# Kernel optimization log

Measured on AMD Instinct MI355X. Metric: run time of the kernel, lower is better.

## Reference

```python
import jax, jax.numpy as jnp
import numpy as np

HIDDEN = 1024
FFN = 4096
NUM_EXPERTS = 8
TOP_K = 2
LOAD_BALANCE_WEIGHT = 0.01


def setup_inputs() -> dict:
    key = jax.random.key(0)
    ks = jax.random.split(key, 6)
    B, S = 4, 2048
    x = jax.random.normal(ks[0], (B, S, HIDDEN), dtype=jnp.float32)
    router_w = jax.random.normal(ks[1], (NUM_EXPERTS, HIDDEN), dtype=jnp.float32) * 0.02
    fc1_w = jax.random.normal(ks[2], (NUM_EXPERTS, FFN, HIDDEN), dtype=jnp.float32) * 0.02
    fc1_b = jnp.zeros((NUM_EXPERTS, FFN), dtype=jnp.float32)
    fc2_w = jax.random.normal(ks[3], (NUM_EXPERTS, HIDDEN, FFN), dtype=jnp.float32) * 0.02
    fc2_b = jnp.zeros((NUM_EXPERTS, HIDDEN), dtype=jnp.float32)
    return {"x": x, "router_w": router_w, "fc1_w": fc1_w, "fc1_b": fc1_b,
            "fc2_w": fc2_w, "fc2_b": fc2_b}


def reference(x, router_w, fc1_w, fc1_b, fc2_w, fc2_b):
    B, S, H = x.shape
    xf = x.reshape(-1, H)                       # [T, H]
    T = xf.shape[0]
    logits = xf @ router_w.T                    # [T, E]
    probs = jax.nn.softmax(logits, axis=-1)
    weights, indices = jax.lax.top_k(probs, TOP_K)   # [T, K]
    weights = weights / jnp.sum(weights, axis=-1, keepdims=True)
    # combine weight per (token, expert): sum of top-k weights assigned to expert
    onehot = jax.nn.one_hot(indices, NUM_EXPERTS, dtype=xf.dtype)  # [T, K, E]
    combine = jnp.sum(weights[..., None] * onehot, axis=1)          # [T, E]
    out = jnp.zeros_like(xf)
    for e in range(NUM_EXPERTS):
        h = jax.nn.gelu(xf @ fc1_w[e].T + fc1_b[e], approximate=False)
        y = h @ fc2_w[e].T + fc2_b[e]
        # tokens not routed to expert e have combine weight 0 -> contribute 0,
        # matching the torch masked gather/scatter-add exactly (dropout in eval).
        out = out + y * combine[:, e:e + 1]
    # load-balance aux loss
    counts = jnp.sum(onehot, axis=(0, 1))                # bincount of indices
    freq = counts / (T * TOP_K)
    aux_loss = LOAD_BALANCE_WEIGHT * NUM_EXPERTS * jnp.sum(jnp.mean(probs, axis=0) * freq)
    return out.reshape(B, S, H), aux_loss
```

## Files before the change

### kernel.cpp

```cpp
#include <hip/hip_runtime.h>
#include <math.h>

#define T_TOK 8192
#define HID 1024
#define FFN_DIM 4096
#define NEXP 8
#define BM 128
#define MAX_TILES 136

typedef __attribute__((ext_vector_type(8))) __bf16 bf16x8;
typedef __attribute__((ext_vector_type(8))) unsigned short ushort8;
typedef __attribute__((ext_vector_type(4))) float f32x4;

static __device__ __forceinline__ unsigned short f2bf(float f) {
  unsigned u = __builtin_bit_cast(unsigned, f);
  u += 0x7FFFu + ((u >> 16) & 1u);
  return (unsigned short)(u >> 16);
}

static __device__ __forceinline__ void gl16(const void* g, void* l) {
  __builtin_amdgcn_global_load_lds((const __attribute__((address_space(1))) unsigned int*)g,
                                   (__attribute__((address_space(3))) unsigned int*)l,
                                   16, 0, 0);
}

static __device__ __forceinline__ ushort8 cvt8(const float* p) {
  float4 a = *(const float4*)p, b = *(const float4*)(p + 4);
  ushort8 o;
  o[0] = f2bf(a.x); o[1] = f2bf(a.y); o[2] = f2bf(a.z); o[3] = f2bf(a.w);
  o[4] = f2bf(b.x); o[5] = f2bf(b.y); o[6] = f2bf(b.z); o[7] = f2bf(b.w);
  return o;
}

__global__ void moe_cvt_x(const float* __restrict__ x, unsigned short* __restrict__ xb) {
  size_t i = ((size_t)blockIdx.x * 256 + threadIdx.x) * 8;
  *(ushort8*)(xb + i) = cvt8(x + i);
}

__global__ void moe_cvt_w(const float* __restrict__ w1, const float* __restrict__ w2,
                          unsigned short* __restrict__ w1b, unsigned short* __restrict__ w2b) {
  size_t i = ((size_t)blockIdx.x * 256 + threadIdx.x) * 8;
  if (blockIdx.y == 0) *(ushort8*)(w1b + i) = cvt8(w1 + i);
  else                 *(ushort8*)(w2b + i) = cvt8(w2 + i);
}

__global__ void moe_router(const float* __restrict__ x, const float* __restrict__ rw,
                           int* __restrict__ tok_idx, float* __restrict__ tok_w,
                           float* __restrict__ pbuf) {
  int t = blockIdx.x * 4 + (threadIdx.x >> 6);
  int lane = threadIdx.x & 63;
  const float* xr = x + (size_t)t * HID;
  double acc[NEXP];
#pragma unroll
  for (int e = 0; e < NEXP; ++e) acc[e] = 0.0;
  for (int i = 0; i < HID / 64; ++i) {
    float xv = xr[lane + 64 * i];
#pragma unroll
    for (int e = 0; e < NEXP; ++e)
      acc[e] += (double)xv * (double)rw[e * HID + lane + 64 * i];
  }
#pragma unroll
  for (int off = 32; off; off >>= 1)
#pragma unroll
    for (int e = 0; e < NEXP; ++e) acc[e] += __shfl_xor(acc[e], off);
  if (lane == 0) {
    double m = acc[0];
#pragma unroll
    for (int e = 1; e < NEXP; ++e) m = acc[e] > m ? acc[e] : m;
    float pf[NEXP], s = 0.0f;
#pragma unroll
    for (int e = 0; e < NEXP; ++e) { pf[e] = expf((float)(acc[e] - m)); s += pf[e]; }
    int i0 = 0;
#pragma unroll
    for (int e = 1; e < NEXP; ++e) if (acc[e] > acc[i0]) i0 = e;
    int i1 = (i0 == 0) ? 1 : 0;
#pragma unroll
    for (int e = 0; e < NEXP; ++e) if (e != i0 && acc[e] > acc[i1]) i1 = e;
    float w0 = pf[i0], w1 = pf[i1], wsum = w0 + w1;
    tok_idx[2 * t] = i0; tok_idx[2 * t + 1] = i1;
    tok_w[2 * t] = w0 / wsum; tok_w[2 * t + 1] = w1 / wsum;
    float inv = 1.0f / s;
#pragma unroll
    for (int e = 0; e < NEXP; ++e) pbuf[(size_t)t * NEXP + e] = pf[e] * inv;
  }
}

__global__ void moe_scatter(const int* __restrict__ tok_idx, const float* __restrict__ tok_w,
                            int* __restrict__ cursor, int* __restrict__ list,
                            float* __restrict__ listw) {
  const int e = blockIdx.x;
  __shared__ int wsum[16];
  __shared__ int base;
  const int tid = threadIdx.x, lane = tid & 63, wv = tid >> 6;
  if (tid == 0) base = 0;
  __syncthreads();
  for (int c = 0; c < 2 * T_TOK; c += 1024) {
    int i = c + tid;
    int m = (tok_idx[i] == e) ? 1 : 0;
    unsigned long long bal = __ballot(m);
    if (lane == 0) wsum[wv] = __popcll(bal);
    __syncthreads();
    int wbase = base;
    for (int k = 0; k < wv; ++k) wbase += wsum[k];
    if (m) {
      int pos = wbase + __popcll(bal & ((1ull << lane) - 1ull));
      list[e * T_TOK + pos] = i >> 1;
      listw[e * T_TOK + pos] = tok_w[i];
    }
    __syncthreads();
    if (tid == 0) {
      int s = 0;
#pragma unroll
      for (int k = 0; k < 16; ++k) s += wsum[k];
      base += s;
    }
    __syncthreads();
  }
  if (tid == 0) cursor[e] = base;
}

__global__ void moe_preduce(const float* __restrict__ pbuf, float* __restrict__ probs_sum) {
  const int e = blockIdx.x;
  float s = 0.0f;
  for (int t = threadIdx.x; t < T_TOK; t += 256) s += pbuf[(size_t)t * NEXP + e];
  __shared__ float red[4];
#pragma unroll
  for (int off = 32; off; off >>= 1) s += __shfl_down(s, off);
  if ((threadIdx.x & 63) == 0) red[threadIdx.x >> 6] = s;
  __syncthreads();
  if (threadIdx.x == 0) probs_sum[e] = red[0] + red[1] + red[2] + red[3];
}

__global__ void moe_offsets(const int* __restrict__ cursor, int* __restrict__ offs,
                            int* __restrict__ tile_e, int* __restrict__ tile_m,
                            int* __restrict__ meta) {
  if (threadIdx.x == 0 && blockIdx.x == 0) {
    int o = 0, t = 0;
    for (int e = 0; e < NEXP; ++e) {
      offs[e] = o;
      int ntl = (cursor[e] + BM - 1) / BM;
      for (int k = 0; k < ntl; ++k) { tile_e[t] = e; tile_m[t] = k; ++t; }
      o += ntl * BM;
    }
    offs[NEXP] = o;
    meta[0] = t;
  }
}

__global__ __launch_bounds__(256, 4) void moe_fc1(
    const unsigned short* __restrict__ xb, const unsigned short* __restrict__ w1b,
    const float* __restrict__ b1, const int* __restrict__ list,
    const int* __restrict__ offs, const int* __restrict__ tile_e,
    const int* __restrict__ tile_m, const int* __restrict__ meta,
    unsigned short* __restrict__ hbuf, int cb, int ch) {
  const int bid = blockIdx.x;
  const int c = bid & 7;
  const int k = bid >> 3;
  const int tl = c * 17 + k % 17;
  const int nt = k / 17;
  if (tl >= meta[0]) return;
  const int e = tile_e[tl], mt = tile_m[tl];
  __shared__ __align__(16) char As[BM * 128];
  __shared__ __align__(16) char Bs[BM * 128];
  const int tid = threadIdx.x, lane = tid & 63, wv = tid >> 6;
  const int wr = wv >> 1, wc = wv & 1;
  const int swz = ((lane & 7) ^ (lane >> 3)) << 4;
  const int rsub = lane >> 3;
  const int* le = list + e * T_TOK + mt * BM;
  const char* asrc[4]; const char* bsrc[4];
  char* adst[4]; char* bdst[4];
#pragma unroll
  for (int j = 0; j < 4; ++j) {
    int r = wv * 32 + j * 8 + rsub;
    int tok = le[r]; tok = tok < 0 ? 0 : tok;
    asrc[j] = (const char*)(xb + (size_t)tok * HID) + swz;
    bsrc[j] = (const char*)(w1b + ((size_t)e * FFN_DIM + cb + nt * BM + r) * HID) + swz;
    adst[j] = As + (wv * 32 + j * 8) * 128;
    bdst[j] = Bs + (wv * 32 + j * 8) * 128;
  }
  f32x4 acc[4][4] = {};
  for (int kt = 0; kt < 16; ++kt) {
    if (kt) __syncthreads();
#pragma unroll
    for (int j = 0; j < 4; ++j) {
      gl16(asrc[j] + kt * 128, adst[j]);
      gl16(bsrc[j] + kt * 128, bdst[j]);
    }
    __syncthreads();
#pragma unroll
    for (int kh = 0; kh < 2; ++kh) {
      bf16x8 afr[4], bfr[4];
      const int kb = kh * 64 + ((lane >> 4) << 4);
#pragma unroll
      for (int m = 0; m < 4; ++m) {
        int row = wr * 64 + m * 16 + (lane & 15);
        afr[m] = *(const bf16x8*)(As + row * 128 + (kb ^ ((row & 7) << 4)));
      }
#pragma unroll
      for (int n = 0; n < 4; ++n) {
        int col = wc * 64 + n * 16 + (lane & 15);
        bfr[n] = *(const bf16x8*)(Bs + col * 128 + (kb ^ ((col & 7) << 4)));
      }
#pragma unroll
      for (int m = 0; m < 4; ++m)
#pragma unroll
        for (int n = 0; n < 4; ++n)
          acc[m][n] = __builtin_amdgcn_mfma_f32_16x16x32_bf16(afr[m], bfr[n], acc[m][n], 0, 0, 0);
    }
  }
  const float* b1e = b1 + (size_t)e * FFN_DIM + cb + nt * BM;
  const size_t rbase = (size_t)(offs[e] + mt * BM);
#pragma unroll
  for (int n = 0; n < 4; ++n) {
    int cl = wc * 64 + n * 16 + (lane & 15);
    float bias = b1e[cl];
#pragma unroll
    for (int m = 0; m < 4; ++m)
#pragma unroll
      for (int j = 0; j < 4; ++j) {
        int rl = wr * 64 + m * 16 + ((lane >> 4) << 2) + j;
        float v = acc[m][n][j] + bias;
        float g = 0.5f * v * (1.0f + erff(v * 0.70710678118654752f));
        hbuf[(rbase + rl) * ch + nt * BM + cl] = f2bf(g);
      }
  }
}

__global__ __launch_bounds__(256, 4) void moe_fc2(
    const unsigned short* __restrict__ hbuf, const unsigned short* __restrict__ w2b,
    const float* __restrict__ b2, const int* __restrict__ list, const float* __restrict__ listw,
    const int* __restrict__ offs, const int* __restrict__ tile_e,
    const int* __restrict__ tile_m, const int* __restrict__ meta,
    float* __restrict__ out, int cb, int ch) {
  const int bid = blockIdx.x;
  const int c = bid & 7;
  const int k = bid >> 3;
  const int tl = c * 17 + (k >> 3);
  const int nt = k & 7;
  if (tl >= meta[0]) return;
  const int e = tile_e[tl], mt = tile_m[tl];
  __shared__ __align__(16) char As[BM * 128];
  __shared__ __align__(16) char Bs[BM * 128];
  const int tid = threadIdx.x, lane = tid & 63, wv = tid >> 6;
  const int wr = wv >> 1, wc = wv & 1;
  const int swz = ((lane & 7) ^ (lane >> 3)) << 4;
  const int rsub = lane >> 3;
  const size_t rbase = (size_t)(offs[e] + mt * BM);
  const char* asrc[4]; const char* bsrc[4];
  char* adst[4]; char* bdst[4];
#pragma unroll
  for (int j = 0; j < 4; ++j) {
    int r = wv * 32 + j * 8 + rsub;
    asrc[j] = (const char*)(hbuf + (rbase + r) * ch) + swz;
    bsrc[j] = (const char*)(w2b + ((size_t)e * HID + nt * BM + r) * FFN_DIM + cb) + swz;
    adst[j] = As + (wv * 32 + j * 8) * 128;
    bdst[j] = Bs + (wv * 32 + j * 8) * 128;
  }
  f32x4 acc[4][4] = {};
  const int nK = ch / 64;
  for (int kt = 0; kt < nK; ++kt) {
    if (kt) __syncthreads();
#pragma unroll
    for (int j = 0; j < 4; ++j) {
      gl16(asrc[j] + kt * 128, adst[j]);
      gl16(bsrc[j] + kt * 128, bdst[j]);
    }
    __syncthreads();
#pragma unroll
    for (int kh = 0; kh < 2; ++kh) {
      bf16x8 afr[4], bfr[4];
      const int kb = kh * 64 + ((lane >> 4) << 4);
#pragma unroll
      for (int m = 0; m < 4; ++m) {
        int row = wr * 64 + m * 16 + (lane & 15);
        afr[m] = *(const bf16x8*)(As + row * 128 + (kb ^ ((row & 7) << 4)));
      }
#pragma unroll
      for (int n = 0; n < 4; ++n) {
        int col = wc * 64 + n * 16 + (lane & 15);
        bfr[n] = *(const bf16x8*)(Bs + col * 128 + (kb ^ ((col & 7) << 4)));
      }
#pragma unroll
      for (int m = 0; m < 4; ++m)
#pragma unroll
        for (int n = 0; n < 4; ++n)
          acc[m][n] = __builtin_amdgcn_mfma_f32_16x16x32_bf16(afr[m], bfr[n], acc[m][n], 0, 0, 0);
    }
  }
  const int* le = list + e * T_TOK + mt * BM;
  const float* lw = listw + e * T_TOK + mt * BM;
  const float* b2e = b2 + (size_t)e * HID + nt * BM;
#pragma unroll
  for (int m = 0; m < 4; ++m)
#pragma unroll
    for (int j = 0; j < 4; ++j) {
      int rl = wr * 64 + m * 16 + ((lane >> 4) << 2) + j;
      int tok = le[rl];
      if (tok < 0) continue;
      float wgt = lw[rl];
      float* orow = out + (size_t)tok * HID + nt * BM;
#pragma unroll
      for (int n = 0; n < 4; ++n) {
        int cl = wc * 64 + n * 16 + (lane & 15);
        float v = acc[m][n][j];
        if (cb == 0) v += b2e[cl];
        atomicAdd(orow + cl, wgt * v);
      }
    }
}

__global__ void moe_finalize(const float* __restrict__ probs_sum, const int* __restrict__ cursor,
                             float* __restrict__ out_aux) {
  if (threadIdx.x == 0 && blockIdx.x == 0) {
    float a = 0.0f;
    for (int e = 0; e < NEXP; ++e)
      a += (probs_sum[e] / (float)T_TOK) * ((float)cursor[e] / (float)(T_TOK * 2));
    out_aux[0] = 0.01f * (float)NEXP * a;
  }
}

extern "C" void kernel_launch(void* const* d_in, const int* in_sizes, int n_in,
                              void* d_out, int out_size, void* d_ws, size_t ws_size,
                              hipStream_t stream) {
  const float* x  = (const float*)d_in[0];
  const float* rw = (const float*)d_in[1];
  const float* w1 = (const float*)d_in[2];
  const float* b1 = (const float*)d_in[3];
  const float* w2 = (const float*)d_in[4];
  const float* b2 = (const float*)d_in[5];
  float* out = (float*)d_out;

  char* ws = (char*)d_ws;
  float* probs_sum = (float*)(ws + 0);
  int*   cursor    = (int*)(ws + 256);
  int*   meta      = (int*)(ws + 512);
  int*   offs      = (int*)(ws + 1024);
  int*   tile_e    = (int*)(ws + 2048);
  int*   tile_m    = (int*)(ws + 4096);
  int*   tok_idx   = (int*)(ws + 8192);
  float* tok_w     = (float*)(ws + 8192 + 65536);
  int*   list      = (int*)(ws + 8192 + 131072);
  float* listw     = (float*)(ws + 8192 + 393216);
  float* pbuf      = (float*)(ws + 8192 + 655360);
  unsigned short* xb   = (unsigned short*)(ws + 1048576);
  unsigned short* w1be = (unsigned short*)(ws + 17825792);
  unsigned short* w2be = (unsigned short*)(ws + 84934656);
  const size_t HBUF_OFF = 152043520;
  unsigned short* hbuf = (unsigned short*)(ws + HBUF_OFF);

  int CH = 4096;
  while (CH > 1024 && HBUF_OFF + (size_t)(MAX_TILES * BM) * CH * 2 > ws_size) CH >>= 1;

  hipMemsetAsync(d_out, 0, (size_t)out_size * sizeof(float), stream);
  hipMemsetAsync(ws + 8192 + 131072, 0xFF, 262144, stream);

  moe_cvt_x<<<4096, 256, 0, stream>>>(x, xb);
  moe_cvt_w<<<dim3(16384, 2), 256, 0, stream>>>(w1, w2, w1be, w2be);
  moe_router<<<T_TOK / 4, 256, 0, stream>>>(x, rw, tok_idx, tok_w, pbuf);
  moe_scatter<<<NEXP, 1024, 0, stream>>>(tok_idx, tok_w, cursor, list, listw);
  moe_preduce<<<NEXP, 256, 0, stream>>>(pbuf, probs_sum);
  moe_offsets<<<1, 1, 0, stream>>>(cursor, offs, tile_e, tile_m, meta);

  for (int cb = 0; cb < FFN_DIM; cb += CH) {
    moe_fc1<<<MAX_TILES * (CH / BM), 256, 0, stream>>>(
        xb, w1be, b1, list, offs, tile_e, tile_m, meta, hbuf, cb, CH);
    moe_fc2<<<MAX_TILES * 8, 256, 0, stream>>>(
        hbuf, w2be, b2, list, listw, offs, tile_e, tile_m, meta, out, cb, CH);
  }
  moe_finalize<<<1, 64, 0, stream>>>(probs_sum, cursor, out + (size_t)T_TOK * HID);
}
```

Measured before the change: 665.9 us.

## Replace fc2 atomic scatter with dense expert output buffer and gather combine

fc2 now writes each expert row's result plainly into a per-expert-row fp32 buffer instead of atomically adding weighted results into the output. A new combine kernel gathers each token's two expert rows through an inverse index and applies the routing weights. The x-to-bf16 conversion is also folded into the router kernel, and the output memset is dropped. This trades atomic contention for an extra ~100MB of buffer traffic and a larger workspace.

```diff
diff --git a/kernel.cpp b/kernel.cpp
--- a/kernel.cpp
+++ b/kernel.cpp
@@ -32,11 +32,6 @@
   return o;
 }
 
-__global__ void moe_cvt_x(const float* __restrict__ x, unsigned short* __restrict__ xb) {
-  size_t i = ((size_t)blockIdx.x * 256 + threadIdx.x) * 8;
-  *(ushort8*)(xb + i) = cvt8(x + i);
-}
-
 __global__ void moe_cvt_w(const float* __restrict__ w1, const float* __restrict__ w2,
                           unsigned short* __restrict__ w1b, unsigned short* __restrict__ w2b) {
   size_t i = ((size_t)blockIdx.x * 256 + threadIdx.x) * 8;
@@ -46,15 +41,17 @@
 
 __global__ void moe_router(const float* __restrict__ x, const float* __restrict__ rw,
                            int* __restrict__ tok_idx, float* __restrict__ tok_w,
-                           float* __restrict__ pbuf) {
+                           float* __restrict__ pbuf, unsigned short* __restrict__ xb) {
   int t = blockIdx.x * 4 + (threadIdx.x >> 6);
   int lane = threadIdx.x & 63;
   const float* xr = x + (size_t)t * HID;
+  unsigned short* xbr = xb + (size_t)t * HID;
   double acc[NEXP];
 #pragma unroll
   for (int e = 0; e < NEXP; ++e) acc[e] = 0.0;
   for (int i = 0; i < HID / 64; ++i) {
     float xv = xr[lane + 64 * i];
+    xbr[lane + 64 * i] = f2bf(xv);
 #pragma unroll
     for (int e = 0; e < NEXP; ++e)
       acc[e] += (double)xv * (double)rw[e * HID + lane + 64 * i];
@@ -85,9 +82,9 @@
   }
 }
 
-__global__ void moe_scatter(const int* __restrict__ tok_idx, const float* __restrict__ tok_w,
+__global__ void moe_scatter(const int* __restrict__ tok_idx,
                             int* __restrict__ cursor, int* __restrict__ list,
-                            float* __restrict__ listw) {
+                            int* __restrict__ inv) {
   const int e = blockIdx.x;
   __shared__ int wsum[16];
   __shared__ int base;
@@ -105,7 +102,7 @@
     if (m) {
       int pos = wbase + __popcll(bal & ((1ull << lane) - 1ull));
       list[e * T_TOK + pos] = i >> 1;
-      listw[e * T_TOK + pos] = tok_w[i];
+      inv[i] = (e << 13) | pos;
     }
     __syncthreads();
     if (tid == 0) {
@@ -228,10 +225,9 @@
 
 __global__ __launch_bounds__(256, 4) void moe_fc2(
     const unsigned short* __restrict__ hbuf, const unsigned short* __restrict__ w2b,
-    const float* __restrict__ b2, const int* __restrict__ list, const float* __restrict__ listw,
-    const int* __restrict__ offs, const int* __restrict__ tile_e,
-    const int* __restrict__ tile_m, const int* __restrict__ meta,
-    float* __restrict__ out, int cb, int ch) {
+    const float* __restrict__ b2, const int* __restrict__ offs,
+    const int* __restrict__ tile_e, const int* __restrict__ tile_m,
+    const int* __restrict__ meta, float* __restrict__ ybuf, int cb, int ch) {
   const int bid = blockIdx.x;
   const int c = bid & 7;
   const int k = bid >> 3;
@@ -287,26 +283,40 @@
           acc[m][n] = __builtin_amdgcn_mfma_f32_16x16x32_bf16(afr[m], bfr[n], acc[m][n], 0, 0, 0);
     }
   }
-  const int* le = list + e * T_TOK + mt * BM;
-  const float* lw = listw + e * T_TOK + mt * BM;
   const float* b2e = b2 + (size_t)e * HID + nt * BM;
 #pragma unroll
   for (int m = 0; m < 4; ++m)
 #pragma unroll
     for (int j = 0; j < 4; ++j) {
       int rl = wr * 64 + m * 16 + ((lane >> 4) << 2) + j;
-      int tok = le[rl];
-      if (tok < 0) continue;
-      float wgt = lw[rl];
-      float* orow = out + (size_t)tok * HID + nt * BM;
+      float* yrow = ybuf + (rbase + rl) * HID + nt * BM;
 #pragma unroll
       for (int n = 0; n < 4; ++n) {
         int cl = wc * 64 + n * 16 + (lane & 15);
         float v = acc[m][n][j];
-        if (cb == 0) v += b2e[cl];
-        atomicAdd(orow + cl, wgt * v);
-      }
-    }
+        if (cb == 0) yrow[cl] = v + b2e[cl];
+        else         yrow[cl] += v;
+      }
+    }
+}
+
+__global__ void moe_combine(const float* __restrict__ ybuf, const int* __restrict__ inv,
+                            const float* __restrict__ tok_w, const int* __restrict__ offs,
+                            float* __restrict__ out) {
+  const int t = blockIdx.x;
+  const int col = threadIdx.x * 4;
+  int v0 = inv[2 * t], v1 = inv[2 * t + 1];
+  size_t r0 = (size_t)(offs[v0 >> 13] + (v0 & 8191));
+  size_t r1 = (size_t)(offs[v1 >> 13] + (v1 & 8191));
+  float w0 = tok_w[2 * t], w1 = tok_w[2 * t + 1];
+  float4 a = *(const float4*)(ybuf + r0 * HID + col);
+  float4 b = *(const float4*)(ybuf + r1 * HID + col);
+  float4 o;
+  o.x = w0 * a.x + w1 * b.x;
+  o.y = w0 * a.y + w1 * b.y;
+  o.z = w0 * a.z + w1 * b.z;
+  o.w = w0 * a.w + w1 * b.w;
+  *(float4*)(out + (size_t)t * HID + col) = o;
 }
 
 __global__ void moe_finalize(const float* __restrict__ probs_sum, const int* __restrict__ cursor,
@@ -340,24 +350,23 @@
   int*   tok_idx   = (int*)(ws + 8192);
   float* tok_w     = (float*)(ws + 8192 + 65536);
   int*   list      = (int*)(ws + 8192 + 131072);
-  float* listw     = (float*)(ws + 8192 + 393216);
   float* pbuf      = (float*)(ws + 8192 + 655360);
+  int*   inv       = (int*)(ws + 925696);
   unsigned short* xb   = (unsigned short*)(ws + 1048576);
   unsigned short* w1be = (unsigned short*)(ws + 17825792);
   unsigned short* w2be = (unsigned short*)(ws + 84934656);
-  const size_t HBUF_OFF = 152043520;
+  float* ybuf = (float*)(ws + 152043520);
+  const size_t HBUF_OFF = 223346688;
   unsigned short* hbuf = (unsigned short*)(ws + HBUF_OFF);
 
   int CH = 4096;
   while (CH > 1024 && HBUF_OFF + (size_t)(MAX_TILES * BM) * CH * 2 > ws_size) CH >>= 1;
 
-  hipMemsetAsync(d_out, 0, (size_t)out_size * sizeof(float), stream);
   hipMemsetAsync(ws + 8192 + 131072, 0xFF, 262144, stream);
 
-  moe_cvt_x<<<4096, 256, 0, stream>>>(x, xb);
   moe_cvt_w<<<dim3(16384, 2), 256, 0, stream>>>(w1, w2, w1be, w2be);
-  moe_router<<<T_TOK / 4, 256, 0, stream>>>(x, rw, tok_idx, tok_w, pbuf);
-  moe_scatter<<<NEXP, 1024, 0, stream>>>(tok_idx, tok_w, cursor, list, listw);
+  moe_router<<<T_TOK / 4, 256, 0, stream>>>(x, rw, tok_idx, tok_w, pbuf, xb);
+  moe_scatter<<<NEXP, 1024, 0, stream>>>(tok_idx, cursor, list, inv);
   moe_preduce<<<NEXP, 256, 0, stream>>>(pbuf, probs_sum);
   moe_offsets<<<1, 1, 0, stream>>>(cursor, offs, tile_e, tile_m, meta);
 
@@ -365,7 +374,8 @@
     moe_fc1<<<MAX_TILES * (CH / BM), 256, 0, stream>>>(
         xb, w1be, b1, list, offs, tile_e, tile_m, meta, hbuf, cb, CH);
     moe_fc2<<<MAX_TILES * 8, 256, 0, stream>>>(
-        hbuf, w2be, b2, list, listw, offs, tile_e, tile_m, meta, out, cb, CH);
-  }
+        hbuf, w2be, b2, offs, tile_e, tile_m, meta, ybuf, cb, CH);
+  }
+  moe_combine<<<T_TOK, 256, 0, stream>>>(ybuf, inv, tok_w, offs, out);
   moe_finalize<<<1, 64, 0, stream>>>(probs_sum, cursor, out + (size_t)T_TOK * HID);
 }
```

After: 607.6 us. 1.1x faster.
